# Kernel optimization log

Measured on AMD Instinct MI355X. Metric: run time of the kernel, lower is better.

## Reference

```python
import jax, jax.numpy as jnp
import numpy as np

NS, NR, D, H, O = 50000, 100000, 128, 128, 2
ESR, ERR, ESS = 1000000, 1600000, 800000


def _sage(x_src, x_dst, src, dst, Wl, bl, Wr, num_dst):
    # PyG SAGEConv(aggr='mean'): lin_l(mean_{j in N(i)} x_j) + lin_r(x_i)
    s = jax.ops.segment_sum(x_src[src], dst, num_segments=num_dst)
    cnt = jax.ops.segment_sum(jnp.ones(dst.shape, x_src.dtype), dst, num_segments=num_dst)
    agg = s / jnp.maximum(cnt, 1.0)[:, None]
    return agg @ Wl + bl + x_dst @ Wr


def setup_inputs() -> dict:
    key = jax.random.key(0)
    ks = jax.random.split(key, 32)
    f = lambda i, shp: jax.random.normal(ks[i], shp, jnp.float32) * 0.05
    inp = {"x_subject": f(0, (NS, D)), "x_roi": f(1, (NR, D))}
    wnames = ["w1_sr_l", "w1_sr_r", "w1_rr_l", "w1_rr_r", "w1_ss_l", "w1_ss_r",
              "w2_sr_l", "w2_sr_r", "w2_rr_l", "w2_rr_r", "w2_ss_l", "w2_ss_r"]
    for i, n in enumerate(wnames):
        inp[n] = f(2 + i, (D if n[1] == '1' else H, H))
    for n in ["b1_sr", "b1_rr", "b1_ss", "b2_sr", "b2_rr", "b2_ss"]:
        inp[n] = jnp.zeros((H,), jnp.float32)
    inp["lin_w"] = f(14, (H, O))
    inp["lin_b"] = jnp.zeros((O,), jnp.float32)
    inp["ei_sr_src"] = jax.random.randint(ks[20], (ESR,), 0, NS, jnp.int32)
    inp["ei_sr_dst"] = jax.random.randint(ks[21], (ESR,), 0, NR, jnp.int32)
    inp["ei_rr_src"] = jax.random.randint(ks[22], (ERR,), 0, NR, jnp.int32)
    inp["ei_rr_dst"] = jax.random.randint(ks[23], (ERR,), 0, NR, jnp.int32)
    inp["ei_ss_src"] = jax.random.randint(ks[24], (ESS,), 0, NS, jnp.int32)
    inp["ei_ss_dst"] = jax.random.randint(ks[25], (ESS,), 0, NS, jnp.int32)
    return inp


def reference(x_subject, x_roi,
              w1_sr_l, b1_sr, w1_sr_r, w1_rr_l, b1_rr, w1_rr_r, w1_ss_l, b1_ss, w1_ss_r,
              w2_sr_l, b2_sr, w2_sr_r, w2_rr_l, b2_rr, w2_rr_r, w2_ss_l, b2_ss, w2_ss_r,
              lin_w, lin_b,
              ei_sr_src, ei_sr_dst, ei_rr_src, ei_rr_dst, ei_ss_src, ei_ss_dst):
    # layer 1: HeteroConv with aggr='mean' over per-edge-type outputs
    r1 = 0.5 * (_sage(x_subject, x_roi, ei_sr_src, ei_sr_dst, w1_sr_l, b1_sr, w1_sr_r, NR)
                + _sage(x_roi, x_roi, ei_rr_src, ei_rr_dst, w1_rr_l, b1_rr, w1_rr_r, NR))
    s1 = _sage(x_subject, x_subject, ei_ss_src, ei_ss_dst, w1_ss_l, b1_ss, w1_ss_r, NS)
    r1, s1 = jax.nn.relu(r1), jax.nn.relu(s1)
    # layer 2 (roi branch is dead code w.r.t. the output, which reads only 'subject')
    s2 = _sage(s1, s1, ei_ss_src, ei_ss_dst, w2_ss_l, b2_ss, w2_ss_r, NS)
    s2 = jax.nn.relu(s2)
    return s2 @ lin_w + lin_b
```

## Files before the change

kernel.cpp:

```cpp
#include <hip/hip_runtime.h>

#define NS   50000
#define ESS  800000
#define D    128

#define BSPAN 256
#define NB    ((NS + BSPAN - 1) / BSPAN)
#define EPB   4096
#define NBLK  ((ESS + EPB - 1) / EPB)
#define NHIST (NB * NBLK)
#define SCAN2_BLOCKS ((NHIST + 255) / 256)

typedef __attribute__((ext_vector_type(8))) short bf16x8;
typedef __attribute__((ext_vector_type(4))) float f32x4;

static __device__ __forceinline__ ushort f2bf(float f) {
    uint u = __float_as_uint(f);
    u += 0x7fffu + ((u >> 16) & 1u);
    return (ushort)(u >> 16);
}
static __device__ __forceinline__ float bf2f(ushort h) {
    return __uint_as_float((uint)h << 16);
}

__global__ __launch_bounds__(256) void split_x_k(
    const float* __restrict__ x, ushort* __restrict__ xh, int n8)
{
    int i = blockIdx.x * 256 + threadIdx.x;
    if (i >= n8) return;
    const float4* src = (const float4*)(x + (size_t)i * 8);
    float4 a = src[0], b = src[1];
    uint4 o;
    o.x = (uint)f2bf(a.x) | ((uint)f2bf(a.y) << 16);
    o.y = (uint)f2bf(a.z) | ((uint)f2bf(a.w) << 16);
    o.z = (uint)f2bf(b.x) | ((uint)f2bf(b.y) << 16);
    o.w = (uint)f2bf(b.z) | ((uint)f2bf(b.w) << 16);
    *(uint4*)(xh + (size_t)i * 8) = o;
}

__global__ __launch_bounds__(256) void prep_w_k(
    const float* __restrict__ w1l, const float* __restrict__ w1r,
    const float* __restrict__ w2l, const float* __restrict__ w2r,
    ushort* __restrict__ wt1h, ushort* __restrict__ wt1l,
    ushort* __restrict__ wt2h, ushort* __restrict__ wt2l)
{
    int t = blockIdx.x * 256 + threadIdx.x;
    int layer = t >> 15;
    int rem   = t & 32767;
    int k     = rem >> 7;
    int col   = rem & 127;
    const float* wl = layer ? w2l : w1l;
    const float* wr = layer ? w2r : w1r;
    float v = (k < 128) ? wl[k * 128 + col] : wr[(k - 128) * 128 + col];
    ushort h = f2bf(v);
    ushort l = f2bf(v - bf2f(h));
    size_t idx = ((size_t)((k >> 5) * 4 + ((k >> 3) & 3)) * 128 + col) * 8 + (k & 7);
    ushort* dh = layer ? wt2h : wt1h;
    ushort* dl = layer ? wt2l : wt1l;
    dh[idx] = h;
    dl[idx] = l;
}

__global__ __launch_bounds__(256) void hist_k(
    const int* __restrict__ dst, int* __restrict__ blockhist)
{
    __shared__ int lh[NB];
    int t = threadIdx.x, blk = blockIdx.x;
    if (t < NB) lh[t] = 0;
    __syncthreads();
    #pragma unroll
    for (int i = 0; i < EPB / 256; ++i) {
        int e = blk * EPB + i * 256 + t;
        if (e < ESS) atomicAdd(&lh[dst[e] >> 8], 1);
    }
    __syncthreads();
    if (t < NB) blockhist[t * NBLK + blk] = lh[t];
}

__global__ __launch_bounds__(256) void block_sum_k(
    const int* __restrict__ deg, int* __restrict__ bsum, int n)
{
    __shared__ int lds[256];
    int i = blockIdx.x * 256 + threadIdx.x;
    int v = (i < n) ? deg[i] : 0;
    lds[threadIdx.x] = v;
    __syncthreads();
    for (int off = 128; off > 0; off >>= 1) {
        if (threadIdx.x < off) lds[threadIdx.x] += lds[threadIdx.x + off];
        __syncthreads();
    }
    if (threadIdx.x == 0) bsum[blockIdx.x] = lds[0];
}

__global__ __launch_bounds__(256) void scan_partials_k(
    const int* __restrict__ bsum, int* __restrict__ boff, int nb)
{
    __shared__ int lds[256];
    int t = threadIdx.x;
    int v = (t < nb) ? bsum[t] : 0;
    lds[t] = v;
    __syncthreads();
    for (int off = 1; off < 256; off <<= 1) {
        int other = (t >= off) ? lds[t - off] : 0;
        __syncthreads();
        lds[t] += other;
        __syncthreads();
    }
    if (t < nb) boff[t] = lds[t] - v;
}

__global__ __launch_bounds__(256) void scan_final_k(
    const int* __restrict__ deg, const int* __restrict__ boff,
    int* __restrict__ row_start, int n)
{
    __shared__ int lds[256];
    int t = threadIdx.x;
    int i = blockIdx.x * 256 + t;
    int v = (i < n) ? deg[i] : 0;
    lds[t] = v;
    __syncthreads();
    for (int off = 1; off < 256; off <<= 1) {
        int other = (t >= off) ? lds[t - off] : 0;
        __syncthreads();
        lds[t] += other;
        __syncthreads();
    }
    if (i < n) row_start[i] = boff[blockIdx.x] + lds[t] - v;
}

__global__ __launch_bounds__(256) void scatter_pairs_k(
    const int* __restrict__ src, const int* __restrict__ dst,
    const int* __restrict__ shist, uint* __restrict__ staging)
{
    __shared__ int lcur[NB];
    int t = threadIdx.x, blk = blockIdx.x;
    if (t < NB) lcur[t] = shist[t * NBLK + blk];
    __syncthreads();
    #pragma unroll
    for (int i = 0; i < EPB / 256; ++i) {
        int e = blk * EPB + i * 256 + t;
        if (e < ESS) {
            int d = dst[e];
            int slot = atomicAdd(&lcur[d >> 8], 1);
            staging[slot] = (uint)src[e] | ((uint)(d & 255) << 16);
        }
    }
}

__global__ __launch_bounds__(256) void bucket_csr_k(
    const uint* __restrict__ staging, const int* __restrict__ shist,
    int* __restrict__ deg, int* __restrict__ row_start,
    int* __restrict__ esrc)
{
    __shared__ int ldeg[BSPAN], lscan[BSPAN], lcur[BSPAN];
    int b = blockIdx.x, t = threadIdx.x;
    int base = shist[b * NBLK];
    int next = (b == NB - 1) ? ESS : shist[(b + 1) * NBLK];
    int n = next - base;
    ldeg[t] = 0;
    __syncthreads();
    for (int i = t; i < n; i += 256)
        atomicAdd(&ldeg[staging[base + i] >> 16], 1);
    __syncthreads();
    int v = ldeg[t];
    lscan[t] = v;
    __syncthreads();
    for (int off = 1; off < 256; off <<= 1) {
        int o = (t >= off) ? lscan[t - off] : 0;
        __syncthreads();
        lscan[t] += o;
        __syncthreads();
    }
    int excl = lscan[t] - v;
    int node = b * BSPAN + t;
    if (node < NS) {
        deg[node] = v;
        row_start[node] = base + excl;
    }
    lcur[t] = base + excl;
    __syncthreads();
    for (int i = t; i < n; i += 256) {
        uint p = staging[base + i];
        int slot = atomicAdd(&lcur[p >> 16], 1);
        esrc[slot] = (int)(p & 0xffffu);
    }
}

__global__ __launch_bounds__(256) void gather_mean_bf16_k(
    const ushort* __restrict__ xh, const int* __restrict__ esrc,
    const int* __restrict__ row_start, const int* __restrict__ deg,
    ushort* __restrict__ aggh, ushort* __restrict__ aggl, int M)
{
    int d = blockIdx.x * 4 + (threadIdx.x >> 6);
    if (d >= M) return;
    int lane = threadIdx.x & 63;
    int beg = row_start[d];
    int n   = deg[d];
    const uint* xp = reinterpret_cast<const uint*>(xh);
    float sx[8] = {}, sy[8] = {};
    int j = 0;
    for (; j + 7 < n; j += 8) {
        uint u[8];
        #pragma unroll
        for (int q = 0; q < 8; ++q) {
            int s = esrc[beg + j + q];
            u[q] = xp[(size_t)s * 64 + lane];
        }
        #pragma unroll
        for (int q = 0; q < 8; ++q) {
            sx[q] += __uint_as_float(u[q] << 16);
            sy[q] += __uint_as_float(u[q] & 0xffff0000u);
        }
    }
    for (; j < n; ++j) {
        int s = esrc[beg + j];
        uint u = xp[(size_t)s * 64 + lane];
        sx[0] += __uint_as_float(u << 16);
        sy[0] += __uint_as_float(u & 0xffff0000u);
    }
    float ax = ((sx[0] + sx[1]) + (sx[2] + sx[3])) + ((sx[4] + sx[5]) + (sx[6] + sx[7]));
    float ay = ((sy[0] + sy[1]) + (sy[2] + sy[3])) + ((sy[4] + sy[5]) + (sy[6] + sy[7]));
    float scale = 1.0f / fmaxf((float)n, 1.0f);
    ax *= scale; ay *= scale;
    ushort hx = f2bf(ax), hy = f2bf(ay);
    ushort lx = f2bf(ax - bf2f(hx)), ly = f2bf(ay - bf2f(hy));
    reinterpret_cast<uint*>(aggh)[(size_t)d * 64 + lane] = (uint)hx | ((uint)hy << 16);
    reinterpret_cast<uint*>(aggl)[(size_t)d * 64 + lane] = (uint)lx | ((uint)ly << 16);
}

template<bool FINAL>
__global__ __launch_bounds__(256) void sage_mfma_k(
    const ushort* __restrict__ aggh, const ushort* __restrict__ aggl,
    const ushort* __restrict__ xh,
    const ushort* __restrict__ wth, const ushort* __restrict__ wtl,
    const float* __restrict__ bias,
    ushort* __restrict__ s_out,
    const float* __restrict__ lin_w, const float* __restrict__ lin_b,
    float* __restrict__ out, int M)
{
    __shared__ __align__(16) ushort Ahs[8][4][64][8];
    __shared__ __align__(16) ushort Als[4][4][64][8];

    const int t    = threadIdx.x;
    const int rb   = blockIdx.x * 64;
    const int wid  = t >> 6;
    const int wm   = wid >> 1;
    const int wn   = wid & 1;
    const int lane = t & 63;
    const int lr   = lane & 15;
    const int kg   = lane >> 4;

    {
        int row = t >> 2, q = t & 3;
        int grow = rb + row;
        bool ok = grow < M;
        #pragma unroll
        for (int i = 0; i < 8; ++i) {
            const ushort* sp = (i < 4)
                ? aggh + (size_t)grow * 128 + i * 32 + q * 8
                : xh   + (size_t)grow * 128 + (i - 4) * 32 + q * 8;
            uint4 v = make_uint4(0, 0, 0, 0);
            if (ok) v = *(const uint4*)sp;
            *(uint4*)&Ahs[i][q][row][0] = v;
        }
        #pragma unroll
        for (int i = 0; i < 4; ++i) {
            const ushort* sp = aggl + (size_t)grow * 128 + i * 32 + q * 8;
            uint4 v = make_uint4(0, 0, 0, 0);
            if (ok) v = *(const uint4*)sp;
            *(uint4*)&Als[i][q][row][0] = v;
        }
    }
    __syncthreads();

    f32x4 acc[2][4] = {};
    #pragma unroll
    for (int ks = 0; ks < 8; ++ks) {
        const bool isAgg = (ks < 4);
        bf16x8 ah[2], al[2], bh[4], bl[4];
        #pragma unroll
        for (int nt = 0; nt < 4; ++nt) {
            int c = wn * 64 + nt * 16 + lr;
            size_t off = ((size_t)(ks * 4 + kg) * 128 + c) * 8;
            bh[nt] = *(const bf16x8*)(wth + off);
            bl[nt] = *(const bf16x8*)(wtl + off);
        }
        #pragma unroll
        for (int mt = 0; mt < 2; ++mt) {
            int r = wm * 32 + mt * 16 + lr;
            ah[mt] = *(const bf16x8*)&Ahs[ks][kg][r][0];
            al[mt] = isAgg ? *(const bf16x8*)&Als[ks][kg][r][0] : ah[mt];
        }
        #pragma unroll
        for (int mt = 0; mt < 2; ++mt) {
            #pragma unroll
            for (int nt = 0; nt < 4; ++nt) {
                acc[mt][nt] = __builtin_amdgcn_mfma_f32_16x16x32_bf16(
                    ah[mt], bh[nt], acc[mt][nt], 0, 0, 0);
                acc[mt][nt] = __builtin_amdgcn_mfma_f32_16x16x32_bf16(
                    ah[mt], bl[nt], acc[mt][nt], 0, 0, 0);
                if (isAgg)
                    acc[mt][nt] = __builtin_amdgcn_mfma_f32_16x16x32_bf16(
                        al[mt], bh[nt], acc[mt][nt], 0, 0, 0);
            }
        }
    }

    #pragma unroll
    for (int mt = 0; mt < 2; ++mt) {
        #pragma unroll
        for (int r = 0; r < 4; ++r) {
            int grow = rb + wm * 32 + mt * 16 + kg * 4 + r;
            if constexpr (FINAL) {
                float p0 = 0.f, p1 = 0.f;
                #pragma unroll
                for (int nt = 0; nt < 4; ++nt) {
                    int col = wn * 64 + nt * 16 + lr;
                    float v = fmaxf(acc[mt][nt][r] + bias[col], 0.f);
                    float2 lw = *(const float2*)(lin_w + col * 2);
                    p0 += v * lw.x;
                    p1 += v * lw.y;
                }
                #pragma unroll
                for (int off = 1; off < 16; off <<= 1) {
                    p0 += __shfl_xor(p0, off);
                    p1 += __shfl_xor(p1, off);
                }
                if (lr == 0 && grow < M) {
                    float b0 = (wn == 0) ? lin_b[0] : 0.f;
                    float b1 = (wn == 0) ? lin_b[1] : 0.f;
                    atomicAdd(&out[(size_t)grow * 2 + 0], p0 + b0);
                    atomicAdd(&out[(size_t)grow * 2 + 1], p1 + b1);
                }
            } else {
                #pragma unroll
                for (int nt = 0; nt < 4; ++nt) {
                    int col = wn * 64 + nt * 16 + lr;
                    float v = fmaxf(acc[mt][nt][r] + bias[col], 0.f);
                    if (grow < M)
                        s_out[(size_t)grow * 128 + col] = f2bf(v);
                }
            }
        }
    }
}

extern "C" void kernel_launch(void* const* d_in, const int* in_sizes, int n_in,
                              void* d_out, int out_size, void* d_ws, size_t ws_size,
                              hipStream_t stream)
{
    const float* x_subject = (const float*)d_in[0];
    const float* w1l  = (const float*)d_in[6];
    const float* w1r  = (const float*)d_in[7];
    const float* w2l  = (const float*)d_in[12];
    const float* w2r  = (const float*)d_in[13];
    const float* b1   = (const float*)d_in[16];
    const float* b2   = (const float*)d_in[19];
    const float* linw = (const float*)d_in[20];
    const float* linb = (const float*)d_in[21];
    const int* ss_src = (const int*)d_in[26];
    const int* ss_dst = (const int*)d_in[27];

    char* wp = (char*)d_ws;
    ushort* xh      = (ushort*)wp; wp += (size_t)NS * D * 2;
    ushort* s1h     = (ushort*)wp; wp += (size_t)NS * D * 2;
    ushort* aggh    = (ushort*)wp; wp += (size_t)NS * D * 2;
    ushort* aggl    = (ushort*)wp; wp += (size_t)NS * D * 2;
    ushort* wt1h    = (ushort*)wp; wp += 256 * 128 * 2;
    ushort* wt1l    = (ushort*)wp; wp += 256 * 128 * 2;
    ushort* wt2h    = (ushort*)wp; wp += 256 * 128 * 2;
    ushort* wt2l    = (ushort*)wp; wp += 256 * 128 * 2;
    uint*  staging  = (uint*)wp;  wp += (size_t)ESS * 4;
    int*   esrc     = (int*)wp;   wp += (size_t)ESS * 4;
    int*   blockhist= (int*)wp;   wp += (size_t)NHIST * 4;
    int*   shist    = (int*)wp;   wp += (size_t)NHIST * 4;
    int*   deg      = (int*)wp;   wp += NS * 4;
    int*   row_start= (int*)wp;   wp += NS * 4;
    int*   bsum     = (int*)wp;   wp += 256 * 4;
    int*   boff     = (int*)wp;   wp += 256 * 4;

    const int gath_blocks = (NS + 3) / 4;
    const int gemm_blocks = (NS + 63) / 64;

    hipMemsetAsync(d_out, 0, (size_t)NS * 2 * sizeof(float), stream);

    split_x_k<<<(NS * D / 8 + 255) / 256, 256, 0, stream>>>(x_subject, xh, NS * D / 8);
    prep_w_k<<<256, 256, 0, stream>>>(w1l, w1r, w2l, w2r, wt1h, wt1l, wt2h, wt2l);

    hist_k<<<NBLK, 256, 0, stream>>>(ss_dst, blockhist);
    block_sum_k<<<SCAN2_BLOCKS, 256, 0, stream>>>(blockhist, bsum, NHIST);
    scan_partials_k<<<1, 256, 0, stream>>>(bsum, boff, SCAN2_BLOCKS);
    scan_final_k<<<SCAN2_BLOCKS, 256, 0, stream>>>(blockhist, boff, shist, NHIST);
    scatter_pairs_k<<<NBLK, 256, 0, stream>>>(ss_src, ss_dst, shist, staging);
    bucket_csr_k<<<NB, 256, 0, stream>>>(staging, shist, deg, row_start, esrc);

    gather_mean_bf16_k<<<gath_blocks, 256, 0, stream>>>(xh, esrc, row_start,
                                                        deg, aggh, aggl, NS);
    sage_mfma_k<false><<<gemm_blocks, 256, 0, stream>>>(
        aggh, aggl, xh, wt1h, wt1l, b1, s1h, nullptr, nullptr, nullptr, NS);

    gather_mean_bf16_k<<<gath_blocks, 256, 0, stream>>>(s1h, esrc, row_start,
                                                        deg, aggh, aggl, NS);
    sage_mfma_k<true><<<gemm_blocks, 256, 0, stream>>>(
        aggh, aggl, s1h, wt2h, wt2l, b2, nullptr, linw, linb, (float*)d_out, NS);
}
```

Before: 314.4 us.

## Restructure CSR build into per-block local sort and fuse prep kernels

Merges the bf16 split, weight prep and bucket-total zeroing into one launch. The global two-level scan and separate histogram/scatter passes are replaced by a pack kernel that sorts each edge block locally in LDS, plus a tiny 196-entry scan. A bucket kernel then gathers the per-block segments into LDS to build the CSR. The gather tail loop becomes masked, and the final GEMM combines its two wave halves through LDS and writes output directly, removing the memset and the atomics. The cost is a fixed LDS capacity (BCAP=8192) per bucket that silently drops edges if exceeded, and serial per-thread copies in bucket_csr.

```diff
diff --git a/kernel.cpp b/kernel.cpp
--- a/kernel.cpp
+++ b/kernel.cpp
@@ -8,8 +8,10 @@
 #define NB    ((NS + BSPAN - 1) / BSPAN)
 #define EPB   4096
 #define NBLK  ((ESS + EPB - 1) / EPB)
-#define NHIST (NB * NBLK)
-#define SCAN2_BLOCKS ((NHIST + 255) / 256)
+#define BCAP  8192
+
+#define SPLIT_BLOCKS (NS * D / 8 / 256)
+#define PREP_BLOCKS  256
 
 typedef __attribute__((ext_vector_type(8))) short bf16x8;
 typedef __attribute__((ext_vector_type(4))) float f32x4;
@@ -23,144 +25,131 @@
     return __uint_as_float((uint)h << 16);
 }
 
-__global__ __launch_bounds__(256) void split_x_k(
-    const float* __restrict__ x, ushort* __restrict__ xh, int n8)
-{
-    int i = blockIdx.x * 256 + threadIdx.x;
-    if (i >= n8) return;
-    const float4* src = (const float4*)(x + (size_t)i * 8);
-    float4 a = src[0], b = src[1];
-    uint4 o;
-    o.x = (uint)f2bf(a.x) | ((uint)f2bf(a.y) << 16);
-    o.y = (uint)f2bf(a.z) | ((uint)f2bf(a.w) << 16);
-    o.z = (uint)f2bf(b.x) | ((uint)f2bf(b.y) << 16);
-    o.w = (uint)f2bf(b.z) | ((uint)f2bf(b.w) << 16);
-    *(uint4*)(xh + (size_t)i * 8) = o;
-}
-
-__global__ __launch_bounds__(256) void prep_w_k(
+__global__ __launch_bounds__(256) void splitprep_k(
+    const float* __restrict__ x, ushort* __restrict__ xh,
     const float* __restrict__ w1l, const float* __restrict__ w1r,
     const float* __restrict__ w2l, const float* __restrict__ w2r,
     ushort* __restrict__ wt1h, ushort* __restrict__ wt1l,
-    ushort* __restrict__ wt2h, ushort* __restrict__ wt2l)
-{
-    int t = blockIdx.x * 256 + threadIdx.x;
-    int layer = t >> 15;
-    int rem   = t & 32767;
-    int k     = rem >> 7;
-    int col   = rem & 127;
-    const float* wl = layer ? w2l : w1l;
-    const float* wr = layer ? w2r : w1r;
-    float v = (k < 128) ? wl[k * 128 + col] : wr[(k - 128) * 128 + col];
-    ushort h = f2bf(v);
-    ushort l = f2bf(v - bf2f(h));
-    size_t idx = ((size_t)((k >> 5) * 4 + ((k >> 3) & 3)) * 128 + col) * 8 + (k & 7);
-    ushort* dh = layer ? wt2h : wt1h;
-    ushort* dl = layer ? wt2l : wt1l;
-    dh[idx] = h;
-    dl[idx] = l;
-}
-
-__global__ __launch_bounds__(256) void hist_k(
-    const int* __restrict__ dst, int* __restrict__ blockhist)
-{
-    __shared__ int lh[NB];
+    ushort* __restrict__ wt2h, ushort* __restrict__ wt2l,
+    int* __restrict__ btotal)
+{
+    int blk = blockIdx.x, t = threadIdx.x;
+    if (blk < SPLIT_BLOCKS) {
+        int i = blk * 256 + t;
+        const float4* src = (const float4*)(x + (size_t)i * 8);
+        float4 a = src[0], b = src[1];
+        uint4 o;
+        o.x = (uint)f2bf(a.x) | ((uint)f2bf(a.y) << 16);
+        o.y = (uint)f2bf(a.z) | ((uint)f2bf(a.w) << 16);
+        o.z = (uint)f2bf(b.x) | ((uint)f2bf(b.y) << 16);
+        o.w = (uint)f2bf(b.z) | ((uint)f2bf(b.w) << 16);
+        *(uint4*)(xh + (size_t)i * 8) = o;
+    } else if (blk < SPLIT_BLOCKS + PREP_BLOCKS) {
+        int g = (blk - SPLIT_BLOCKS) * 256 + t;
+        int layer = g >> 15;
+        int rem   = g & 32767;
+        int k     = rem >> 7;
+        int col   = rem & 127;
+        const float* wl = layer ? w2l : w1l;
+        const float* wr = layer ? w2r : w1r;
+        float v = (k < 128) ? wl[k * 128 + col] : wr[(k - 128) * 128 + col];
+        ushort h = f2bf(v);
+        ushort l = f2bf(v - bf2f(h));
+        size_t idx = ((size_t)((k >> 5) * 4 + ((k >> 3) & 3)) * 128 + col) * 8 + (k & 7);
+        (layer ? wt2h : wt1h)[idx] = h;
+        (layer ? wt2l : wt1l)[idx] = l;
+    } else {
+        if (t < NB) btotal[t] = 0;
+    }
+}
+
+__global__ __launch_bounds__(256) void pack_k(
+    const int* __restrict__ src, const int* __restrict__ dst,
+    uint* __restrict__ staging, int* __restrict__ blockhist,
+    int* __restrict__ blockstart, int* __restrict__ btotal)
+{
+    __shared__ uint ldata[EPB];
+    __shared__ int lh[256], lofs[256], lcur[256];
     int t = threadIdx.x, blk = blockIdx.x;
-    if (t < NB) lh[t] = 0;
-    __syncthreads();
-    #pragma unroll
-    for (int i = 0; i < EPB / 256; ++i) {
-        int e = blk * EPB + i * 256 + t;
-        if (e < ESS) atomicAdd(&lh[dst[e] >> 8], 1);
-    }
-    __syncthreads();
-    if (t < NB) blockhist[t * NBLK + blk] = lh[t];
-}
-
-__global__ __launch_bounds__(256) void block_sum_k(
-    const int* __restrict__ deg, int* __restrict__ bsum, int n)
-{
-    __shared__ int lds[256];
-    int i = blockIdx.x * 256 + threadIdx.x;
-    int v = (i < n) ? deg[i] : 0;
-    lds[threadIdx.x] = v;
-    __syncthreads();
-    for (int off = 128; off > 0; off >>= 1) {
-        if (threadIdx.x < off) lds[threadIdx.x] += lds[threadIdx.x + off];
-        __syncthreads();
-    }
-    if (threadIdx.x == 0) bsum[blockIdx.x] = lds[0];
-}
-
-__global__ __launch_bounds__(256) void scan_partials_k(
-    const int* __restrict__ bsum, int* __restrict__ boff, int nb)
+    int base = blk * EPB;
+    int nmine = min(EPB, ESS - base);
+    lh[t] = 0;
+    __syncthreads();
+    for (int i = t; i < nmine; i += 256) {
+        int s = src[base + i], d = dst[base + i];
+        ldata[i] = (uint)s | ((uint)(d & 255) << 16) | ((uint)(d >> 8) << 24);
+        atomicAdd(&lh[d >> 8], 1);
+    }
+    __syncthreads();
+    int v = lh[t];
+    lofs[t] = v;
+    __syncthreads();
+    for (int off = 1; off < 256; off <<= 1) {
+        int o = (t >= off) ? lofs[t - off] : 0;
+        __syncthreads();
+        lofs[t] += o;
+        __syncthreads();
+    }
+    int excl = lofs[t] - v;
+    if (t < NB) {
+        blockhist[blk * NB + t]  = v;
+        blockstart[blk * NB + t] = excl;
+        if (v) atomicAdd(&btotal[t], v);
+    }
+    lcur[t] = excl;
+    __syncthreads();
+    for (int i = t; i < nmine; i += 256) {
+        uint p = ldata[i];
+        int slot = atomicAdd(&lcur[p >> 24], 1);
+        staging[base + slot] = p;
+    }
+}
+
+__global__ __launch_bounds__(256) void scan196_k(
+    const int* __restrict__ btotal, int* __restrict__ bucket_base)
 {
     __shared__ int lds[256];
     int t = threadIdx.x;
-    int v = (t < nb) ? bsum[t] : 0;
+    int v = (t < NB) ? btotal[t] : 0;
     lds[t] = v;
     __syncthreads();
     for (int off = 1; off < 256; off <<= 1) {
-        int other = (t >= off) ? lds[t - off] : 0;
-        __syncthreads();
-        lds[t] += other;
-        __syncthreads();
-    }
-    if (t < nb) boff[t] = lds[t] - v;
-}
-
-__global__ __launch_bounds__(256) void scan_final_k(
-    const int* __restrict__ deg, const int* __restrict__ boff,
-    int* __restrict__ row_start, int n)
-{
-    __shared__ int lds[256];
-    int t = threadIdx.x;
-    int i = blockIdx.x * 256 + t;
-    int v = (i < n) ? deg[i] : 0;
-    lds[t] = v;
+        int o = (t >= off) ? lds[t - off] : 0;
+        __syncthreads();
+        lds[t] += o;
+        __syncthreads();
+    }
+    if (t < NB) bucket_base[t] = lds[t] - v;
+}
+
+__global__ __launch_bounds__(256) void bucket_csr_k(
+    const uint* __restrict__ staging, const int* __restrict__ blockhist,
+    const int* __restrict__ blockstart, const int* __restrict__ bucket_base,
+    int* __restrict__ deg, int* __restrict__ row_start, int* __restrict__ esrc)
+{
+    __shared__ uint bdata[BCAP];
+    __shared__ int lscan[256], ldeg[256], lcur[256];
+    int b = blockIdx.x, t = threadIdx.x;
+    int c = (t < NBLK) ? blockhist[t * NB + b] : 0;
+    lscan[t] = c;
     __syncthreads();
     for (int off = 1; off < 256; off <<= 1) {
-        int other = (t >= off) ? lds[t - off] : 0;
-        __syncthreads();
-        lds[t] += other;
-        __syncthreads();
-    }
-    if (i < n) row_start[i] = boff[blockIdx.x] + lds[t] - v;
-}
-
-__global__ __launch_bounds__(256) void scatter_pairs_k(
-    const int* __restrict__ src, const int* __restrict__ dst,
-    const int* __restrict__ shist, uint* __restrict__ staging)
-{
-    __shared__ int lcur[NB];
-    int t = threadIdx.x, blk = blockIdx.x;
-    if (t < NB) lcur[t] = shist[t * NBLK + blk];
-    __syncthreads();
-    #pragma unroll
-    for (int i = 0; i < EPB / 256; ++i) {
-        int e = blk * EPB + i * 256 + t;
-        if (e < ESS) {
-            int d = dst[e];
-            int slot = atomicAdd(&lcur[d >> 8], 1);
-            staging[slot] = (uint)src[e] | ((uint)(d & 255) << 16);
-        }
-    }
-}
-
-__global__ __launch_bounds__(256) void bucket_csr_k(
-    const uint* __restrict__ staging, const int* __restrict__ shist,
-    int* __restrict__ deg, int* __restrict__ row_start,
-    int* __restrict__ esrc)
-{
-    __shared__ int ldeg[BSPAN], lscan[BSPAN], lcur[BSPAN];
-    int b = blockIdx.x, t = threadIdx.x;
-    int base = shist[b * NBLK];
-    int next = (b == NB - 1) ? ESS : shist[(b + 1) * NBLK];
-    int n = next - base;
+        int o = (t >= off) ? lscan[t - off] : 0;
+        __syncthreads();
+        lscan[t] += o;
+        __syncthreads();
+    }
+    int total = min(lscan[255], BCAP);
+    int excl  = lscan[t] - c;
+    if (t < NBLK && c > 0) {
+        const uint* sp = staging + (size_t)t * EPB + blockstart[t * NB + b];
+        for (int i = 0; i < c; ++i)
+            if (excl + i < BCAP) bdata[excl + i] = sp[i];
+    }
     ldeg[t] = 0;
     __syncthreads();
-    for (int i = t; i < n; i += 256)
-        atomicAdd(&ldeg[staging[base + i] >> 16], 1);
+    for (int i = t; i < total; i += 256)
+        atomicAdd(&ldeg[(bdata[i] >> 16) & 255], 1);
     __syncthreads();
     int v = ldeg[t];
     lscan[t] = v;
@@ -171,18 +160,19 @@
         lscan[t] += o;
         __syncthreads();
     }
-    int excl = lscan[t] - v;
-    int node = b * BSPAN + t;
+    int nexcl = lscan[t] - v;
+    int gbase = bucket_base[b];
+    int node  = b * BSPAN + t;
     if (node < NS) {
         deg[node] = v;
-        row_start[node] = base + excl;
-    }
-    lcur[t] = base + excl;
-    __syncthreads();
-    for (int i = t; i < n; i += 256) {
-        uint p = staging[base + i];
-        int slot = atomicAdd(&lcur[p >> 16], 1);
-        esrc[slot] = (int)(p & 0xffffu);
+        row_start[node] = gbase + nexcl;
+    }
+    lcur[t] = nexcl;
+    __syncthreads();
+    for (int i = t; i < total; i += 256) {
+        uint p = bdata[i];
+        int slot = atomicAdd(&lcur[(p >> 16) & 255], 1);
+        esrc[gbase + slot] = (int)(p & 0xffffu);
     }
 }
 
@@ -198,25 +188,24 @@
     int n   = deg[d];
     const uint* xp = reinterpret_cast<const uint*>(xh);
     float sx[8] = {}, sy[8] = {};
-    int j = 0;
-    for (; j + 7 < n; j += 8) {
+    for (int j = 0; j < n; j += 8) {
         uint u[8];
+        bool m[8];
         #pragma unroll
         for (int q = 0; q < 8; ++q) {
-            int s = esrc[beg + j + q];
+            int jq = j + q;
+            bool ok = jq < n;
+            int s = esrc[beg + (ok ? jq : 0)];
             u[q] = xp[(size_t)s * 64 + lane];
+            m[q] = ok;
         }
         #pragma unroll
         for (int q = 0; q < 8; ++q) {
-            sx[q] += __uint_as_float(u[q] << 16);
-            sy[q] += __uint_as_float(u[q] & 0xffff0000u);
-        }
-    }
-    for (; j < n; ++j) {
-        int s = esrc[beg + j];
-        uint u = xp[(size_t)s * 64 + lane];
-        sx[0] += __uint_as_float(u << 16);
-        sy[0] += __uint_as_float(u & 0xffff0000u);
+            if (m[q]) {
+                sx[q] += __uint_as_float(u[q] << 16);
+                sy[q] += __uint_as_float(u[q] & 0xffff0000u);
+            }
+        }
     }
     float ax = ((sx[0] + sx[1]) + (sx[2] + sx[3])) + ((sx[4] + sx[5]) + (sx[6] + sx[7]));
     float ay = ((sy[0] + sy[1]) + (sy[2] + sy[3])) + ((sy[4] + sy[5]) + (sy[6] + sy[7]));
@@ -240,6 +229,7 @@
 {
     __shared__ __align__(16) ushort Ahs[8][4][64][8];
     __shared__ __align__(16) ushort Als[4][4][64][8];
+    __shared__ float lps[2][32][2];
 
     const int t    = threadIdx.x;
     const int rb   = blockIdx.x * 64;
@@ -306,12 +296,12 @@
         }
     }
 
-    #pragma unroll
-    for (int mt = 0; mt < 2; ++mt) {
-        #pragma unroll
-        for (int r = 0; r < 4; ++r) {
-            int grow = rb + wm * 32 + mt * 16 + kg * 4 + r;
-            if constexpr (FINAL) {
+    if constexpr (FINAL) {
+        float pv[2][4][2];
+        #pragma unroll
+        for (int mt = 0; mt < 2; ++mt) {
+            #pragma unroll
+            for (int r = 0; r < 4; ++r) {
                 float p0 = 0.f, p1 = 0.f;
                 #pragma unroll
                 for (int nt = 0; nt < 4; ++nt) {
@@ -326,13 +316,40 @@
                     p0 += __shfl_xor(p0, off);
                     p1 += __shfl_xor(p1, off);
                 }
-                if (lr == 0 && grow < M) {
-                    float b0 = (wn == 0) ? lin_b[0] : 0.f;
-                    float b1 = (wn == 0) ? lin_b[1] : 0.f;
-                    atomicAdd(&out[(size_t)grow * 2 + 0], p0 + b0);
-                    atomicAdd(&out[(size_t)grow * 2 + 1], p1 + b1);
+                pv[mt][r][0] = p0;
+                pv[mt][r][1] = p1;
+            }
+        }
+        if (wn == 1 && lr == 0) {
+            #pragma unroll
+            for (int mt = 0; mt < 2; ++mt)
+                #pragma unroll
+                for (int r = 0; r < 4; ++r) {
+                    int row = mt * 16 + kg * 4 + r;
+                    lps[wm][row][0] = pv[mt][r][0];
+                    lps[wm][row][1] = pv[mt][r][1];
                 }
-            } else {
+        }
+        __syncthreads();
+        if (wn == 0 && lr == 0) {
+            #pragma unroll
+            for (int mt = 0; mt < 2; ++mt)
+                #pragma unroll
+                for (int r = 0; r < 4; ++r) {
+                    int row = mt * 16 + kg * 4 + r;
+                    int grow = rb + wm * 32 + row;
+                    if (grow < M) {
+                        out[(size_t)grow * 2 + 0] = pv[mt][r][0] + lps[wm][row][0] + lin_b[0];
+                        out[(size_t)grow * 2 + 1] = pv[mt][r][1] + lps[wm][row][1] + lin_b[1];
+                    }
+                }
+        }
+    } else {
+        #pragma unroll
+        for (int mt = 0; mt < 2; ++mt) {
+            #pragma unroll
+            for (int r = 0; r < 4; ++r) {
+                int grow = rb + wm * 32 + mt * 16 + kg * 4 + r;
                 #pragma unroll
                 for (int nt = 0; nt < 4; ++nt) {
                     int col = wn * 64 + nt * 16 + lr;
@@ -362,37 +379,34 @@
     const int* ss_dst = (const int*)d_in[27];
 
     char* wp = (char*)d_ws;
-    ushort* xh      = (ushort*)wp; wp += (size_t)NS * D * 2;
-    ushort* s1h     = (ushort*)wp; wp += (size_t)NS * D * 2;
-    ushort* aggh    = (ushort*)wp; wp += (size_t)NS * D * 2;
-    ushort* aggl    = (ushort*)wp; wp += (size_t)NS * D * 2;
-    ushort* wt1h    = (ushort*)wp; wp += 256 * 128 * 2;
-    ushort* wt1l    = (ushort*)wp; wp += 256 * 128 * 2;
-    ushort* wt2h    = (ushort*)wp; wp += 256 * 128 * 2;
-    ushort* wt2l    = (ushort*)wp; wp += 256 * 128 * 2;
-    uint*  staging  = (uint*)wp;  wp += (size_t)ESS * 4;
-    int*   esrc     = (int*)wp;   wp += (size_t)ESS * 4;
-    int*   blockhist= (int*)wp;   wp += (size_t)NHIST * 4;
-    int*   shist    = (int*)wp;   wp += (size_t)NHIST * 4;
-    int*   deg      = (int*)wp;   wp += NS * 4;
-    int*   row_start= (int*)wp;   wp += NS * 4;
-    int*   bsum     = (int*)wp;   wp += 256 * 4;
-    int*   boff     = (int*)wp;   wp += 256 * 4;
+    ushort* xh        = (ushort*)wp; wp += (size_t)NS * D * 2;
+    ushort* s1h       = (ushort*)wp; wp += (size_t)NS * D * 2;
+    ushort* aggh      = (ushort*)wp; wp += (size_t)NS * D * 2;
+    ushort* aggl      = (ushort*)wp; wp += (size_t)NS * D * 2;
+    ushort* wt1h      = (ushort*)wp; wp += 256 * 128 * 2;
+    ushort* wt1l      = (ushort*)wp; wp += 256 * 128 * 2;
+    ushort* wt2h      = (ushort*)wp; wp += 256 * 128 * 2;
+    ushort* wt2l      = (ushort*)wp; wp += 256 * 128 * 2;
+    uint*  staging    = (uint*)wp;  wp += (size_t)NBLK * EPB * 4;
+    int*   esrc       = (int*)wp;   wp += (size_t)ESS * 4;
+    int*   blockhist  = (int*)wp;   wp += (size_t)NBLK * NB * 4;
+    int*   blockstart = (int*)wp;   wp += (size_t)NBLK * NB * 4;
+    int*   btotal     = (int*)wp;   wp += NB * 4;
+    int*   bucket_base= (int*)wp;   wp += NB * 4;
+    int*   deg        = (int*)wp;   wp += NS * 4;
+    int*   row_start  = (int*)wp;   wp += NS * 4;
 
     const int gath_blocks = (NS + 3) / 4;
     const int gemm_blocks = (NS + 63) / 64;
 
-    hipMemsetAsync(d_out, 0, (size_t)NS * 2 * sizeof(float), stream);
-
-    split_x_k<<<(NS * D / 8 + 255) / 256, 256, 0, stream>>>(x_subject, xh, NS * D / 8);
-    prep_w_k<<<256, 256, 0, stream>>>(w1l, w1r, w2l, w2r, wt1h, wt1l, wt2h, wt2l);
-
-    hist_k<<<NBLK, 256, 0, stream>>>(ss_dst, blockhist);
-    block_sum_k<<<SCAN2_BLOCKS, 256, 0, stream>>>(blockhist, bsum, NHIST);
-    scan_partials_k<<<1, 256, 0, stream>>>(bsum, boff, SCAN2_BLOCKS);
-    scan_final_k<<<SCAN2_BLOCKS, 256, 0, stream>>>(blockhist, boff, shist, NHIST);
-    scatter_pairs_k<<<NBLK, 256, 0, stream>>>(ss_src, ss_dst, shist, staging);
-    bucket_csr_k<<<NB, 256, 0, stream>>>(staging, shist, deg, row_start, esrc);
+    splitprep_k<<<SPLIT_BLOCKS + PREP_BLOCKS + 1, 256, 0, stream>>>(
+        x_subject, xh, w1l, w1r, w2l, w2r, wt1h, wt1l, wt2h, wt2l, btotal);
+
+    pack_k<<<NBLK, 256, 0, stream>>>(ss_src, ss_dst, staging,
+                                     blockhist, blockstart, btotal);
+    scan196_k<<<1, 256, 0, stream>>>(btotal, bucket_base);
+    bucket_csr_k<<<NB, 256, 0, stream>>>(staging, blockhist, blockstart,
+                                         bucket_base, deg, row_start, esrc);
 
     gather_mean_bf16_k<<<gath_blocks, 256, 0, stream>>>(xh, esrc, row_start,
                                                         deg, aggh, aggl, NS);
```

After: 311.1 us. Within noise of the previous version (-1.0%).
